# Performance work log

Measured on AMD Instinct MI355X. Metric: run time of the kernel, lower is better.

Reference implementation:

```python
import jax, jax.numpy as jnp
import numpy as np

U, P, D, H, E = 512, 1024, 128, 256, 98304
N = U + P


def setup_inputs() -> dict:
    key = jax.random.key(0)
    ks = jax.random.split(key, 16)
    def nrm(k, shape, scale=0.05):
        return jax.random.normal(k, shape, jnp.float32) * scale
    z = lambda *s: jnp.zeros(s, jnp.float32)
    return {
        "user_ids": jnp.arange(U),
        "paper_ids": jnp.arange(P),
        "edge_index": jax.random.randint(ks[0], (2, E), 0, N),
        "user_paper_interactions": jax.random.uniform(ks[1], (U, P), jnp.float32),
        "user_emb": nrm(ks[2], (U, D), 1.0),   # nn.Embedding tables
        "paper_emb": nrm(ks[3], (P, D), 1.0),
        "W0": nrm(ks[4], (D, H)), "b0": z(H),   # GCNConv weights (stored [in,out])
        "W1": nrm(ks[5], (H, H)), "b1": z(H),
        "W2": nrm(ks[6], (H, H)), "b2": z(H),
        "Wu": nrm(ks[7], (H, D)), "bu": z(D),   # user_output Linear
        "Wp": nrm(ks[8], (H, D)), "bp": z(D),   # paper_output Linear
        "Wq1": nrm(ks[9], (2 * D, H)), "bq1": z(H),  # predictor Linear 1
        "Wq2": nrm(ks[10], (H, 1)), "bq2": z(1),      # predictor Linear 2
    }


def gcn_conv(x, src, dst, W, b):
    """PyG GCNConv: add self-loops, symmetric D^-1/2 (A+I) D^-1/2 normalization."""
    n = x.shape[0]
    loop = jnp.arange(n)
    s = jnp.concatenate([src, loop])
    d = jnp.concatenate([dst, loop])
    deg = jax.ops.segment_sum(jnp.ones(d.shape, x.dtype), d, num_segments=n)
    dis = jnp.where(deg > 0, jax.lax.rsqrt(jnp.maximum(deg, 1.0)), 0.0)
    norm = dis[s] * dis[d]                      # [E+n]
    h = x @ W                                   # [n, H]
    out = jax.ops.segment_sum(h[s] * norm[:, None], d, num_segments=n)
    return out + b


def reference(user_ids, paper_ids, edge_index, user_paper_interactions,
              user_emb, paper_emb, W0, b0, W1, b1, W2, b2,
              Wu, bu, Wp, bp, Wq1, bq1, Wq2, bq2):
    # embedding lookups + node feature matrix [U+P, D]
    x = jnp.concatenate([user_emb[user_ids], paper_emb[paper_ids]], axis=0)
    src, dst = edge_index[0], edge_index[1]
    for W, b in ((W0, b0), (W1, b1), (W2, b2)):
        x = jax.nn.relu(gcn_conv(x, src, dst, W, b))  # dropout is identity in eval
    nu = user_ids.shape[0]
    np_ = paper_ids.shape[0]
    user_final = x[:nu] @ Wu + bu               # [U, D]
    paper_final = x[nu:] @ Wp + bp              # [P, D]
    # broadcast outer-product concat -> [U, P, 2D]
    combined = jnp.concatenate([
        jnp.broadcast_to(user_final[:, None, :], (nu, np_, user_final.shape[-1])),
        jnp.broadcast_to(paper_final[None, :, :], (nu, np_, paper_final.shape[-1])),
    ], axis=-1)
    h = jax.nn.relu(combined @ Wq1 + bq1)       # [U, P, H]
    pred = jax.nn.sigmoid(h @ Wq2 + bq2)[..., 0]  # [U, P]
    return pred
```

## Files before the change

kernel.cpp:

```cpp
#include <hip/hip_runtime.h>
#include <math.h>

constexpr int Uc = 512;
constexpr int Pc = 1024;
constexpr int Dc = 128;
constexpr int Hc = 256;
constexpr int Ec = 98304;
constexpr int Nc = 1536;
constexpr int CAP = 192;

__device__ __forceinline__ void fma4(float4& a, float n, const float4 r) {
    a.x += n * r.x; a.y += n * r.y; a.z += n * r.z; a.w += n * r.w;
}

template <int K>
__device__ __forceinline__ void gemm_core16(const float* __restrict__ xr,
                                            const float* __restrict__ wc, int M,
                                            float& acc0, float& acc1) {
#pragma unroll 4
    for (int k = 0; k < K; k += 4) {
        float4 a = *(const float4*)(xr + k);
        float2 b0 = *(const float2*)(wc + (size_t)k * M);
        float2 b1 = *(const float2*)(wc + (size_t)(k + 1) * M);
        float2 b2 = *(const float2*)(wc + (size_t)(k + 2) * M);
        float2 b3 = *(const float2*)(wc + (size_t)(k + 3) * M);
        acc0 += a.x * b0.x; acc1 += a.x * b0.y;
        acc0 += a.y * b1.x; acc1 += a.y * b1.y;
        acc0 += a.z * b2.x; acc1 += a.z * b2.y;
        acc0 += a.w * b3.x; acc1 += a.w * b3.y;
    }
}

__global__ void k_front(const int* __restrict__ e_src, const int* __restrict__ e_dst,
                        int* __restrict__ cnt, int* __restrict__ colF,
                        const float* __restrict__ Wu, const float* __restrict__ Wp,
                        const float* __restrict__ Wq1, const float* __restrict__ bu,
                        const float* __restrict__ bp, const float* __restrict__ bq1,
                        float* __restrict__ Wup, float* __restrict__ Wpp,
                        float* __restrict__ bvu, float* __restrict__ bvp) {
    int t = threadIdx.x, b = blockIdx.x;
    if (b < 384) {
        int e = b * 256 + t;
        int d = e_dst[e];
        int pos = atomicAdd(&cnt[d], 1);
        if (pos < CAP) colF[d * CAP + pos] = e_src[e];
    } else if (b < 640) {
        int id = b - 384;
        int z = id >> 7, tile = id & 127;
        int tx = t & 15, ty = t >> 4;
        const float* X = z ? Wp : Wu;
        const float* W = Wq1 + (z ? (size_t)Dc * Hc : 0);
        float* Y = z ? Wpp : Wup;
        int row = (tile >> 3) * 16 + ty, col = (tile & 7) * 32 + tx * 2;
        float a0 = 0.f, a1 = 0.f;
        gemm_core16<Dc>(X + (size_t)row * Dc, W + col, Hc, a0, a1);
        *(float2*)&Y[(size_t)row * Hc + col] = make_float2(a0, a1);
    } else if (b == 640) {
        float s = bq1[t];
#pragma unroll 8
        for (int d = 0; d < Dc; d++) s += bu[d] * Wq1[d * Hc + t];
        bvu[t] = s;
    } else {
        float s = 0.f;
#pragma unroll 8
        for (int d = 0; d < Dc; d++) s += bp[d] * Wq1[(Dc + d) * Hc + t];
        bvp[t] = s;
    }
}

__global__ void k_l0(const int* __restrict__ uid, const int* __restrict__ pid,
                     const float* __restrict__ ue, const float* __restrict__ pe,
                     const float* __restrict__ W0, const float* __restrict__ b0,
                     const int* __restrict__ cnt, const int* __restrict__ colF,
                     float* __restrict__ out) {
    __shared__ const float* sptr[4][CAP];
    __shared__ float snrm[4][CAP];
    __shared__ __align__(16) float agg[4][Dc];
    int t = threadIdx.x, b = blockIdx.x;
    int ibase = b * 4;
    int c[4]; float di[4];
#pragma unroll
    for (int r = 0; r < 4; r++) {
        c[r] = cnt[ibase + r];
        di[r] = rsqrtf((float)(c[r] + 1));
        int deg = min(c[r], CAP);
        if (t < deg) {
            int s = colF[(ibase + r) * CAP + t];
            sptr[r][t] = (s < Uc) ? ue + (size_t)uid[s] * Dc
                                  : pe + (size_t)pid[s - Uc] * Dc;
            snrm[r][t] = rsqrtf((float)(cnt[s] + 1));
        }
    }
    __syncthreads();
    {
        int wv = t >> 6, ln = t & 63;
        int i = ibase + wv;
        int dg = min(c[wv], CAP);
        const float* xi = (i < Uc) ? ue + (size_t)uid[i] * Dc
                                   : pe + (size_t)pid[i - Uc] * Dc;
        float2 a2 = *(const float2*)(xi + ln * 2);
        float2 acc = make_float2(di[wv] * a2.x, di[wv] * a2.y);
        int j = 0;
        for (; j + 4 <= dg; j += 4) {
            float n0 = snrm[wv][j],     n1 = snrm[wv][j + 1];
            float n2 = snrm[wv][j + 2], n3 = snrm[wv][j + 3];
            float2 r0 = *(const float2*)(sptr[wv][j] + ln * 2);
            float2 r1 = *(const float2*)(sptr[wv][j + 1] + ln * 2);
            float2 r2 = *(const float2*)(sptr[wv][j + 2] + ln * 2);
            float2 r3 = *(const float2*)(sptr[wv][j + 3] + ln * 2);
            acc.x += n0 * r0.x + n1 * r1.x + n2 * r2.x + n3 * r3.x;
            acc.y += n0 * r0.y + n1 * r1.y + n2 * r2.y + n3 * r3.y;
        }
        for (; j < dg; j++) {
            float2 r0 = *(const float2*)(sptr[wv][j] + ln * 2);
            acc.x += snrm[wv][j] * r0.x;
            acc.y += snrm[wv][j] * r0.y;
        }
        agg[wv][ln * 2]     = di[wv] * acc.x;
        agg[wv][ln * 2 + 1] = di[wv] * acc.y;
    }
    __syncthreads();
    float a0 = 0.f, a1 = 0.f, a2 = 0.f, a3 = 0.f;
#pragma unroll 2
    for (int k = 0; k < Dc; k += 4) {
        float4 g0 = *(const float4*)&agg[0][k];
        float4 g1 = *(const float4*)&agg[1][k];
        float4 g2 = *(const float4*)&agg[2][k];
        float4 g3 = *(const float4*)&agg[3][k];
        float w0 = W0[(size_t)(k + 0) * Hc + t];
        float w1 = W0[(size_t)(k + 1) * Hc + t];
        float w2 = W0[(size_t)(k + 2) * Hc + t];
        float w3 = W0[(size_t)(k + 3) * Hc + t];
        a0 += g0.x * w0 + g0.y * w1 + g0.z * w2 + g0.w * w3;
        a1 += g1.x * w0 + g1.y * w1 + g1.z * w2 + g1.w * w3;
        a2 += g2.x * w0 + g2.y * w1 + g2.z * w2 + g2.w * w3;
        a3 += g3.x * w0 + g3.y * w1 + g3.z * w2 + g3.w * w3;
    }
    float bb = b0[t];
    out[(size_t)(ibase + 0) * Hc + t] = fmaxf(a0 + bb, 0.f);
    out[(size_t)(ibase + 1) * Hc + t] = fmaxf(a1 + bb, 0.f);
    out[(size_t)(ibase + 2) * Hc + t] = fmaxf(a2 + bb, 0.f);
    out[(size_t)(ibase + 3) * Hc + t] = fmaxf(a3 + bb, 0.f);
}

__device__ __forceinline__ void agg_wave(const float* __restrict__ X,
                                         const int (*sidx)[CAP], const float (*snrm)[CAP],
                                         const int* c, const float* di, int ibase,
                                         float (*agg)[Hc], int t) {
    int wv = t >> 6, ln = t & 63;
    int dg = min(c[wv], CAP);
    float4 acc = *(const float4*)&X[(size_t)(ibase + wv) * Hc + ln * 4];
    acc.x *= di[wv]; acc.y *= di[wv]; acc.z *= di[wv]; acc.w *= di[wv];
    int j = 0;
    for (; j + 4 <= dg; j += 4) {
        float n0 = snrm[wv][j],     n1 = snrm[wv][j + 1];
        float n2 = snrm[wv][j + 2], n3 = snrm[wv][j + 3];
        float4 r0 = *(const float4*)&X[sidx[wv][j]     + ln * 4];
        float4 r1 = *(const float4*)&X[sidx[wv][j + 1] + ln * 4];
        float4 r2 = *(const float4*)&X[sidx[wv][j + 2] + ln * 4];
        float4 r3 = *(const float4*)&X[sidx[wv][j + 3] + ln * 4];
        fma4(acc, n0, r0); fma4(acc, n1, r1); fma4(acc, n2, r2); fma4(acc, n3, r3);
    }
    for (; j < dg; j++) {
        float4 r0 = *(const float4*)&X[sidx[wv][j] + ln * 4];
        fma4(acc, snrm[wv][j], r0);
    }
    acc.x *= di[wv]; acc.y *= di[wv]; acc.z *= di[wv]; acc.w *= di[wv];
    *(float4*)&agg[wv][ln * 4] = acc;
}

__global__ void k_lh(const float* __restrict__ X, const float* __restrict__ W,
                     const float* __restrict__ bias, const int* __restrict__ cnt,
                     const int* __restrict__ colF, float* __restrict__ out) {
    __shared__ int sidx[4][CAP];
    __shared__ float snrm[4][CAP];
    __shared__ __align__(16) float agg[4][Hc];
    int t = threadIdx.x, b = blockIdx.x;
    int ibase = b * 4;
    int c[4]; float di[4];
#pragma unroll
    for (int r = 0; r < 4; r++) {
        c[r] = cnt[ibase + r];
        di[r] = rsqrtf((float)(c[r] + 1));
        int deg = min(c[r], CAP);
        if (t < deg) {
            int s = colF[(ibase + r) * CAP + t];
            sidx[r][t] = s * Hc;
            snrm[r][t] = rsqrtf((float)(cnt[s] + 1));
        }
    }
    __syncthreads();
    agg_wave(X, sidx, snrm, c, di, ibase, agg, t);
    __syncthreads();
    float a0 = 0.f, a1 = 0.f, a2 = 0.f, a3 = 0.f;
#pragma unroll 2
    for (int k = 0; k < Hc; k += 4) {
        float4 g0 = *(const float4*)&agg[0][k];
        float4 g1 = *(const float4*)&agg[1][k];
        float4 g2 = *(const float4*)&agg[2][k];
        float4 g3 = *(const float4*)&agg[3][k];
        float w0 = W[(size_t)(k + 0) * Hc + t];
        float w1 = W[(size_t)(k + 1) * Hc + t];
        float w2 = W[(size_t)(k + 2) * Hc + t];
        float w3 = W[(size_t)(k + 3) * Hc + t];
        a0 += g0.x * w0 + g0.y * w1 + g0.z * w2 + g0.w * w3;
        a1 += g1.x * w0 + g1.y * w1 + g1.z * w2 + g1.w * w3;
        a2 += g2.x * w0 + g2.y * w1 + g2.z * w2 + g2.w * w3;
        a3 += g3.x * w0 + g3.y * w1 + g3.z * w2 + g3.w * w3;
    }
    float bb = bias[t];
    out[(size_t)(ibase + 0) * Hc + t] = fmaxf(a0 + bb, 0.f);
    out[(size_t)(ibase + 1) * Hc + t] = fmaxf(a1 + bb, 0.f);
    out[(size_t)(ibase + 2) * Hc + t] = fmaxf(a2 + bb, 0.f);
    out[(size_t)(ibase + 3) * Hc + t] = fmaxf(a3 + bb, 0.f);
}

__global__ void k_lht(const float* __restrict__ X, const float* __restrict__ W2,
                      const float* __restrict__ b2, const int* __restrict__ cnt,
                      const int* __restrict__ colF,
                      const float* __restrict__ Wup, const float* __restrict__ Wpp,
                      const float* __restrict__ bvu, const float* __restrict__ bvp,
                      float* __restrict__ AuT, float* __restrict__ ApT) {
    __shared__ int sidx[4][CAP];
    __shared__ float snrm[4][CAP];
    __shared__ __align__(16) float agg[4][Hc];
    __shared__ __align__(16) float xloc[4][Hc];
    int t = threadIdx.x, b = blockIdx.x;
    int ibase = b * 4;
    int c[4]; float di[4];
#pragma unroll
    for (int r = 0; r < 4; r++) {
        c[r] = cnt[ibase + r];
        di[r] = rsqrtf((float)(c[r] + 1));
        int deg = min(c[r], CAP);
        if (t < deg) {
            int s = colF[(ibase + r) * CAP + t];
            sidx[r][t] = s * Hc;
            snrm[r][t] = rsqrtf((float)(cnt[s] + 1));
        }
    }
    __syncthreads();
    agg_wave(X, sidx, snrm, c, di, ibase, agg, t);
    __syncthreads();
    {
        float a0 = 0.f, a1 = 0.f, a2 = 0.f, a3 = 0.f;
#pragma unroll 2
        for (int k = 0; k < Hc; k += 4) {
            float4 g0 = *(const float4*)&agg[0][k];
            float4 g1 = *(const float4*)&agg[1][k];
            float4 g2 = *(const float4*)&agg[2][k];
            float4 g3 = *(const float4*)&agg[3][k];
            float w0 = W2[(size_t)(k + 0) * Hc + t];
            float w1 = W2[(size_t)(k + 1) * Hc + t];
            float w2 = W2[(size_t)(k + 2) * Hc + t];
            float w3 = W2[(size_t)(k + 3) * Hc + t];
            a0 += g0.x * w0 + g0.y * w1 + g0.z * w2 + g0.w * w3;
            a1 += g1.x * w0 + g1.y * w1 + g1.z * w2 + g1.w * w3;
            a2 += g2.x * w0 + g2.y * w1 + g2.z * w2 + g2.w * w3;
            a3 += g3.x * w0 + g3.y * w1 + g3.z * w2 + g3.w * w3;
        }
        float bb = b2[t];
        xloc[0][t] = fmaxf(a0 + bb, 0.f);
        xloc[1][t] = fmaxf(a1 + bb, 0.f);
        xloc[2][t] = fmaxf(a2 + bb, 0.f);
        xloc[3][t] = fmaxf(a3 + bb, 0.f);
    }
    __syncthreads();
    {
        const float* Wsel = (b < 128) ? Wup : Wpp;
        const float* bsel = (b < 128) ? bvu : bvp;
        float* YT  = (b < 128) ? AuT : ApT;
        int ldy    = (b < 128) ? Uc : Pc;
        int rloc   = (b < 128) ? ibase : ibase - Uc;
        float a0 = 0.f, a1 = 0.f, a2 = 0.f, a3 = 0.f;
#pragma unroll 2
        for (int k = 0; k < Hc; k += 4) {
            float4 g0 = *(const float4*)&xloc[0][k];
            float4 g1 = *(const float4*)&xloc[1][k];
            float4 g2 = *(const float4*)&xloc[2][k];
            float4 g3 = *(const float4*)&xloc[3][k];
            float w0 = Wsel[(size_t)(k + 0) * Hc + t];
            float w1 = Wsel[(size_t)(k + 1) * Hc + t];
            float w2 = Wsel[(size_t)(k + 2) * Hc + t];
            float w3 = Wsel[(size_t)(k + 3) * Hc + t];
            a0 += g0.x * w0 + g0.y * w1 + g0.z * w2 + g0.w * w3;
            a1 += g1.x * w0 + g1.y * w1 + g1.z * w2 + g1.w * w3;
            a2 += g2.x * w0 + g2.y * w1 + g2.z * w2 + g2.w * w3;
            a3 += g3.x * w0 + g3.y * w1 + g3.z * w2 + g3.w * w3;
        }
        float bb = bsel[t];
        float4 o = make_float4(a0 + bb, a1 + bb, a2 + bb, a3 + bb);
        *(float4*)&YT[(size_t)t * ldy + rloc] = o;
    }
}

__global__ void k_pred(const float* __restrict__ AuT, const float* __restrict__ ApT,
                       const float* __restrict__ Wq2, const float* __restrict__ bq2,
                       float* __restrict__ out) {
    __shared__ float auS[Hc * 16];
    int t = threadIdx.x;
    int ub = blockIdx.x * 16, pb = blockIdx.y * 64;
#pragma unroll
    for (int i = t; i < Hc * 16; i += 256) {
        int k = i >> 4, u = i & 15;
        auS[i] = AuT[(size_t)k * Uc + ub + u];
    }
    __syncthreads();
    int uu = t >> 5;
    int pp = t & 31;
    const float* app = ApT + pb + pp * 2;
    const float* aup = auS + uu * 2;
    float acc[2][2] = {};
#pragma unroll 4
    for (int k = 0; k < Hc; k += 4) {
        float4 wv = *(const float4*)&Wq2[k];
        float2 a[4], p2[4];
#pragma unroll
        for (int j = 0; j < 4; j++) a[j] = *(const float2*)(aup + (k + j) * 16);
#pragma unroll
        for (int j = 0; j < 4; j++) p2[j] = *(const float2*)(app + (size_t)(k + j) * Pc);
        const float* w = (const float*)&wv;
#pragma unroll
        for (int j = 0; j < 4; j++) {
            float a0 = a[j].x, a1 = a[j].y;
            float p0 = p2[j].x, p1 = p2[j].y;
            acc[0][0] += fmaxf(a0 + p0, 0.f) * w[j];
            acc[0][1] += fmaxf(a0 + p1, 0.f) * w[j];
            acc[1][0] += fmaxf(a1 + p0, 0.f) * w[j];
            acc[1][1] += fmaxf(a1 + p1, 0.f) * w[j];
        }
    }
    float bq = bq2[0];
#pragma unroll
    for (int r = 0; r < 2; r++) {
        int u = ub + uu * 2 + r;
        float2 o;
        o.x = 1.f / (1.f + __expf(-(acc[r][0] + bq)));
        o.y = 1.f / (1.f + __expf(-(acc[r][1] + bq)));
        *(float2*)&out[(size_t)u * Pc + pb + pp * 2] = o;
    }
}


extern "C" void kernel_launch(void* const* d_in, const int* in_sizes, int n_in,
                              void* d_out, int out_size, void* d_ws, size_t ws_size,
                              hipStream_t stream) {
    const int*   uid = (const int*)d_in[0];
    const int*   pid = (const int*)d_in[1];
    const int*   ei  = (const int*)d_in[2];
    const float* ue  = (const float*)d_in[4];
    const float* pe  = (const float*)d_in[5];
    const float* W0  = (const float*)d_in[6];  const float* b0 = (const float*)d_in[7];
    const float* W1  = (const float*)d_in[8];  const float* b1 = (const float*)d_in[9];
    const float* W2  = (const float*)d_in[10]; const float* b2 = (const float*)d_in[11];
    const float* Wu  = (const float*)d_in[12]; const float* bu = (const float*)d_in[13];
    const float* Wp  = (const float*)d_in[14]; const float* bp = (const float*)d_in[15];
    const float* Wq1 = (const float*)d_in[16]; const float* bq1 = (const float*)d_in[17];
    const float* Wq2 = (const float*)d_in[18]; const float* bq2 = (const float*)d_in[19];

    const int* e_src = ei;
    const int* e_dst = ei + Ec;

    char* w = (char*)d_ws;
    auto alloc = [&](size_t bytes) { char* p = w; w += (bytes + 255) & ~size_t(255); return p; };
    int*   cnt  = (int*)alloc(Nc * 4);
    int*   colF = (int*)alloc((size_t)Nc * CAP * 4);
    float* xA   = (float*)alloc((size_t)Nc * Hc * 4);
    float* xB   = (float*)alloc((size_t)Nc * Hc * 4);
    float* Wup  = (float*)alloc((size_t)Hc * Hc * 4);
    float* Wpp  = (float*)alloc((size_t)Hc * Hc * 4);
    float* bvu  = (float*)alloc(Hc * 4);
    float* bvp  = (float*)alloc(Hc * 4);
    float* AuT  = (float*)alloc((size_t)Hc * Uc * 4);
    float* ApT  = (float*)alloc((size_t)Hc * Pc * 4);
    float* pred = (float*)d_out;

    hipMemsetAsync(cnt, 0, Nc * 4, stream);
    k_front<<<642, 256, 0, stream>>>(e_src, e_dst, cnt, colF, Wu, Wp, Wq1,
                                     bu, bp, bq1, Wup, Wpp, bvu, bvp);
    k_l0<<<Nc / 4, 256, 0, stream>>>(uid, pid, ue, pe, W0, b0, cnt, colF, xA);
    k_lh<<<Nc / 4, 256, 0, stream>>>(xA, W1, b1, cnt, colF, xB);
    k_lht<<<Nc / 4, 256, 0, stream>>>(xB, W2, b2, cnt, colF, Wup, Wpp, bvu, bvp, AuT, ApT);
    k_pred<<<dim3(Uc / 16, Pc / 64), 256, 0, stream>>>(AuT, ApT, Wq2, bq2, pred);
}
```

Measured before the change: 204.1 us.

## Split neighbor aggregation across two waves per node, halve nodes per block

GCN layer kernels now process two nodes per block instead of four, with two waves splitting each node's neighbor list and reducing partial sums through shared memory. This doubles the block count and the waves in flight for the latency-bound gather. In exchange, weight rows are reused across fewer nodes in the fused GEMM, and an extra shared-memory reduction and barrier are added.

```diff
diff --git a/kernel.cpp b/kernel.cpp
--- a/kernel.cpp
+++ b/kernel.cpp
@@ -73,14 +73,15 @@
                      const float* __restrict__ W0, const float* __restrict__ b0,
                      const int* __restrict__ cnt, const int* __restrict__ colF,
                      float* __restrict__ out) {
-    __shared__ const float* sptr[4][CAP];
-    __shared__ float snrm[4][CAP];
-    __shared__ __align__(16) float agg[4][Dc];
+    __shared__ const float* sptr[2][CAP];
+    __shared__ float snrm[2][CAP];
+    __shared__ __align__(16) float pagg[4][Dc];
+    __shared__ __align__(16) float agg[2][Dc];
     int t = threadIdx.x, b = blockIdx.x;
-    int ibase = b * 4;
-    int c[4]; float di[4];
-#pragma unroll
-    for (int r = 0; r < 4; r++) {
+    int ibase = b * 2;
+    int c[2]; float di[2];
+#pragma unroll
+    for (int r = 0; r < 2; r++) {
         c[r] = cnt[ibase + r];
         di[r] = rsqrtf((float)(c[r] + 1));
         int deg = min(c[r], CAP);
@@ -94,92 +95,104 @@
     __syncthreads();
     {
         int wv = t >> 6, ln = t & 63;
-        int i = ibase + wv;
-        int dg = min(c[wv], CAP);
-        const float* xi = (i < Uc) ? ue + (size_t)uid[i] * Dc
-                                   : pe + (size_t)pid[i - Uc] * Dc;
-        float2 a2 = *(const float2*)(xi + ln * 2);
-        float2 acc = make_float2(di[wv] * a2.x, di[wv] * a2.y);
-        int j = 0;
-        for (; j + 4 <= dg; j += 4) {
-            float n0 = snrm[wv][j],     n1 = snrm[wv][j + 1];
-            float n2 = snrm[wv][j + 2], n3 = snrm[wv][j + 3];
-            float2 r0 = *(const float2*)(sptr[wv][j] + ln * 2);
-            float2 r1 = *(const float2*)(sptr[wv][j + 1] + ln * 2);
-            float2 r2 = *(const float2*)(sptr[wv][j + 2] + ln * 2);
-            float2 r3 = *(const float2*)(sptr[wv][j + 3] + ln * 2);
+        int r = wv >> 1, h = wv & 1;
+        int i = ibase + r;
+        int dg = min(c[r], CAP);
+        int dg2 = dg >> 1;
+        int j0 = h ? dg2 : 0, j1 = h ? dg : dg2;
+        float2 acc = make_float2(0.f, 0.f);
+        if (h == 0) {
+            const float* xi = (i < Uc) ? ue + (size_t)uid[i] * Dc
+                                       : pe + (size_t)pid[i - Uc] * Dc;
+            float2 a2 = *(const float2*)(xi + ln * 2);
+            acc.x = di[r] * a2.x;
+            acc.y = di[r] * a2.y;
+        }
+        int j = j0;
+        for (; j + 4 <= j1; j += 4) {
+            float n0 = snrm[r][j],     n1 = snrm[r][j + 1];
+            float n2 = snrm[r][j + 2], n3 = snrm[r][j + 3];
+            float2 r0 = *(const float2*)(sptr[r][j] + ln * 2);
+            float2 r1 = *(const float2*)(sptr[r][j + 1] + ln * 2);
+            float2 r2 = *(const float2*)(sptr[r][j + 2] + ln * 2);
+            float2 r3 = *(const float2*)(sptr[r][j + 3] + ln * 2);
             acc.x += n0 * r0.x + n1 * r1.x + n2 * r2.x + n3 * r3.x;
             acc.y += n0 * r0.y + n1 * r1.y + n2 * r2.y + n3 * r3.y;
         }
-        for (; j < dg; j++) {
-            float2 r0 = *(const float2*)(sptr[wv][j] + ln * 2);
-            acc.x += snrm[wv][j] * r0.x;
-            acc.y += snrm[wv][j] * r0.y;
-        }
-        agg[wv][ln * 2]     = di[wv] * acc.x;
-        agg[wv][ln * 2 + 1] = di[wv] * acc.y;
-    }
-    __syncthreads();
-    float a0 = 0.f, a1 = 0.f, a2 = 0.f, a3 = 0.f;
+        for (; j < j1; j++) {
+            float2 r0 = *(const float2*)(sptr[r][j] + ln * 2);
+            acc.x += snrm[r][j] * r0.x;
+            acc.y += snrm[r][j] * r0.y;
+        }
+        pagg[wv][ln * 2]     = acc.x;
+        pagg[wv][ln * 2 + 1] = acc.y;
+    }
+    __syncthreads();
+    {
+        int r = t >> 7, f = t & 127;
+        agg[r][f] = di[r] * (pagg[2 * r][f] + pagg[2 * r + 1][f]);
+    }
+    __syncthreads();
+    float a0 = 0.f, a1 = 0.f;
 #pragma unroll 2
     for (int k = 0; k < Dc; k += 4) {
         float4 g0 = *(const float4*)&agg[0][k];
         float4 g1 = *(const float4*)&agg[1][k];
-        float4 g2 = *(const float4*)&agg[2][k];
-        float4 g3 = *(const float4*)&agg[3][k];
         float w0 = W0[(size_t)(k + 0) * Hc + t];
         float w1 = W0[(size_t)(k + 1) * Hc + t];
         float w2 = W0[(size_t)(k + 2) * Hc + t];
         float w3 = W0[(size_t)(k + 3) * Hc + t];
         a0 += g0.x * w0 + g0.y * w1 + g0.z * w2 + g0.w * w3;
         a1 += g1.x * w0 + g1.y * w1 + g1.z * w2 + g1.w * w3;
-        a2 += g2.x * w0 + g2.y * w1 + g2.z * w2 + g2.w * w3;
-        a3 += g3.x * w0 + g3.y * w1 + g3.z * w2 + g3.w * w3;
     }
     float bb = b0[t];
     out[(size_t)(ibase + 0) * Hc + t] = fmaxf(a0 + bb, 0.f);
     out[(size_t)(ibase + 1) * Hc + t] = fmaxf(a1 + bb, 0.f);
-    out[(size_t)(ibase + 2) * Hc + t] = fmaxf(a2 + bb, 0.f);
-    out[(size_t)(ibase + 3) * Hc + t] = fmaxf(a3 + bb, 0.f);
-}
-
-__device__ __forceinline__ void agg_wave(const float* __restrict__ X,
-                                         const int (*sidx)[CAP], const float (*snrm)[CAP],
-                                         const int* c, const float* di, int ibase,
-                                         float (*agg)[Hc], int t) {
+}
+
+__device__ __forceinline__ void agg_wave2(const float* __restrict__ X,
+                                          const int (*sidx)[CAP], const float (*snrm)[CAP],
+                                          const int* c, const float* di, int ibase,
+                                          float (*pagg)[Hc], int t) {
     int wv = t >> 6, ln = t & 63;
-    int dg = min(c[wv], CAP);
-    float4 acc = *(const float4*)&X[(size_t)(ibase + wv) * Hc + ln * 4];
-    acc.x *= di[wv]; acc.y *= di[wv]; acc.z *= di[wv]; acc.w *= di[wv];
-    int j = 0;
-    for (; j + 4 <= dg; j += 4) {
-        float n0 = snrm[wv][j],     n1 = snrm[wv][j + 1];
-        float n2 = snrm[wv][j + 2], n3 = snrm[wv][j + 3];
-        float4 r0 = *(const float4*)&X[sidx[wv][j]     + ln * 4];
-        float4 r1 = *(const float4*)&X[sidx[wv][j + 1] + ln * 4];
-        float4 r2 = *(const float4*)&X[sidx[wv][j + 2] + ln * 4];
-        float4 r3 = *(const float4*)&X[sidx[wv][j + 3] + ln * 4];
+    int r = wv >> 1, h = wv & 1;
+    int dg = min(c[r], CAP);
+    int dg2 = dg >> 1;
+    int j0 = h ? dg2 : 0, j1 = h ? dg : dg2;
+    float4 acc = make_float4(0.f, 0.f, 0.f, 0.f);
+    if (h == 0) {
+        acc = *(const float4*)&X[(size_t)(ibase + r) * Hc + ln * 4];
+        acc.x *= di[r]; acc.y *= di[r]; acc.z *= di[r]; acc.w *= di[r];
+    }
+    int j = j0;
+    for (; j + 4 <= j1; j += 4) {
+        float n0 = snrm[r][j],     n1 = snrm[r][j + 1];
+        float n2 = snrm[r][j + 2], n3 = snrm[r][j + 3];
+        float4 r0 = *(const float4*)&X[sidx[r][j]     + ln * 4];
+        float4 r1 = *(const float4*)&X[sidx[r][j + 1] + ln * 4];
+        float4 r2 = *(const float4*)&X[sidx[r][j + 2] + ln * 4];
+        float4 r3 = *(const float4*)&X[sidx[r][j + 3] + ln * 4];
         fma4(acc, n0, r0); fma4(acc, n1, r1); fma4(acc, n2, r2); fma4(acc, n3, r3);
     }
-    for (; j < dg; j++) {
-        float4 r0 = *(const float4*)&X[sidx[wv][j] + ln * 4];
-        fma4(acc, snrm[wv][j], r0);
-    }
-    acc.x *= di[wv]; acc.y *= di[wv]; acc.z *= di[wv]; acc.w *= di[wv];
-    *(float4*)&agg[wv][ln * 4] = acc;
+    for (; j < j1; j++) {
+        float4 r0 = *(const float4*)&X[sidx[r][j] + ln * 4];
+        fma4(acc, snrm[r][j], r0);
+    }
+    *(float4*)&pagg[wv][ln * 4] = acc;
 }
 
 __global__ void k_lh(const float* __restrict__ X, const float* __restrict__ W,
                      const float* __restrict__ bias, const int* __restrict__ cnt,
                      const int* __restrict__ colF, float* __restrict__ out) {
-    __shared__ int sidx[4][CAP];
-    __shared__ float snrm[4][CAP];
-    __shared__ __align__(16) float agg[4][Hc];
+    __shared__ int sidx[2][CAP];
+    __shared__ float snrm[2][CAP];
+    __shared__ __align__(16) float pagg[4][Hc];
+    __shared__ __align__(16) float agg[2][Hc];
     int t = threadIdx.x, b = blockIdx.x;
-    int ibase = b * 4;
-    int c[4]; float di[4];
-#pragma unroll
-    for (int r = 0; r < 4; r++) {
+    int ibase = b * 2;
+    int c[2]; float di[2];
+#pragma unroll
+    for (int r = 0; r < 2; r++) {
         c[r] = cnt[ibase + r];
         di[r] = rsqrtf((float)(c[r] + 1));
         int deg = min(c[r], CAP);
@@ -190,29 +203,26 @@
         }
     }
     __syncthreads();
-    agg_wave(X, sidx, snrm, c, di, ibase, agg, t);
-    __syncthreads();
-    float a0 = 0.f, a1 = 0.f, a2 = 0.f, a3 = 0.f;
+    agg_wave2(X, sidx, snrm, c, di, ibase, pagg, t);
+    __syncthreads();
+    agg[0][t] = di[0] * (pagg[0][t] + pagg[1][t]);
+    agg[1][t] = di[1] * (pagg[2][t] + pagg[3][t]);
+    __syncthreads();
+    float a0 = 0.f, a1 = 0.f;
 #pragma unroll 2
     for (int k = 0; k < Hc; k += 4) {
         float4 g0 = *(const float4*)&agg[0][k];
         float4 g1 = *(const float4*)&agg[1][k];
-        float4 g2 = *(const float4*)&agg[2][k];
-        float4 g3 = *(const float4*)&agg[3][k];
         float w0 = W[(size_t)(k + 0) * Hc + t];
         float w1 = W[(size_t)(k + 1) * Hc + t];
         float w2 = W[(size_t)(k + 2) * Hc + t];
         float w3 = W[(size_t)(k + 3) * Hc + t];
         a0 += g0.x * w0 + g0.y * w1 + g0.z * w2 + g0.w * w3;
         a1 += g1.x * w0 + g1.y * w1 + g1.z * w2 + g1.w * w3;
-        a2 += g2.x * w0 + g2.y * w1 + g2.z * w2 + g2.w * w3;
-        a3 += g3.x * w0 + g3.y * w1 + g3.z * w2 + g3.w * w3;
     }
     float bb = bias[t];
     out[(size_t)(ibase + 0) * Hc + t] = fmaxf(a0 + bb, 0.f);
     out[(size_t)(ibase + 1) * Hc + t] = fmaxf(a1 + bb, 0.f);
-    out[(size_t)(ibase + 2) * Hc + t] = fmaxf(a2 + bb, 0.f);
-    out[(size_t)(ibase + 3) * Hc + t] = fmaxf(a3 + bb, 0.f);
 }
 
 __global__ void k_lht(const float* __restrict__ X, const float* __restrict__ W2,
@@ -221,15 +231,16 @@
                       const float* __restrict__ Wup, const float* __restrict__ Wpp,
                       const float* __restrict__ bvu, const float* __restrict__ bvp,
                       float* __restrict__ AuT, float* __restrict__ ApT) {
-    __shared__ int sidx[4][CAP];
-    __shared__ float snrm[4][CAP];
-    __shared__ __align__(16) float agg[4][Hc];
-    __shared__ __align__(16) float xloc[4][Hc];
+    __shared__ int sidx[2][CAP];
+    __shared__ float snrm[2][CAP];
+    __shared__ __align__(16) float pagg[4][Hc];
+    __shared__ __align__(16) float agg[2][Hc];
+    __shared__ __align__(16) float xloc[2][Hc];
     int t = threadIdx.x, b = blockIdx.x;
-    int ibase = b * 4;
-    int c[4]; float di[4];
-#pragma unroll
-    for (int r = 0; r < 4; r++) {
+    int ibase = b * 2;
+    int c[2]; float di[2];
+#pragma unroll
+    for (int r = 0; r < 2; r++) {
         c[r] = cnt[ibase + r];
         di[r] = rsqrtf((float)(c[r] + 1));
         int deg = min(c[r], CAP);
@@ -240,57 +251,49 @@
         }
     }
     __syncthreads();
-    agg_wave(X, sidx, snrm, c, di, ibase, agg, t);
+    agg_wave2(X, sidx, snrm, c, di, ibase, pagg, t);
+    __syncthreads();
+    agg[0][t] = di[0] * (pagg[0][t] + pagg[1][t]);
+    agg[1][t] = di[1] * (pagg[2][t] + pagg[3][t]);
     __syncthreads();
     {
-        float a0 = 0.f, a1 = 0.f, a2 = 0.f, a3 = 0.f;
+        float a0 = 0.f, a1 = 0.f;
 #pragma unroll 2
         for (int k = 0; k < Hc; k += 4) {
             float4 g0 = *(const float4*)&agg[0][k];
             float4 g1 = *(const float4*)&agg[1][k];
-            float4 g2 = *(const float4*)&agg[2][k];
-            float4 g3 = *(const float4*)&agg[3][k];
             float w0 = W2[(size_t)(k + 0) * Hc + t];
             float w1 = W2[(size_t)(k + 1) * Hc + t];
             float w2 = W2[(size_t)(k + 2) * Hc + t];
             float w3 = W2[(size_t)(k + 3) * Hc + t];
             a0 += g0.x * w0 + g0.y * w1 + g0.z * w2 + g0.w * w3;
             a1 += g1.x * w0 + g1.y * w1 + g1.z * w2 + g1.w * w3;
-            a2 += g2.x * w0 + g2.y * w1 + g2.z * w2 + g2.w * w3;
-            a3 += g3.x * w0 + g3.y * w1 + g3.z * w2 + g3.w * w3;
         }
         float bb = b2[t];
         xloc[0][t] = fmaxf(a0 + bb, 0.f);
         xloc[1][t] = fmaxf(a1 + bb, 0.f);
-        xloc[2][t] = fmaxf(a2 + bb, 0.f);
-        xloc[3][t] = fmaxf(a3 + bb, 0.f);
     }
     __syncthreads();
     {
-        const float* Wsel = (b < 128) ? Wup : Wpp;
-        const float* bsel = (b < 128) ? bvu : bvp;
-        float* YT  = (b < 128) ? AuT : ApT;
-        int ldy    = (b < 128) ? Uc : Pc;
-        int rloc   = (b < 128) ? ibase : ibase - Uc;
-        float a0 = 0.f, a1 = 0.f, a2 = 0.f, a3 = 0.f;
+        const float* Wsel = (b < 256) ? Wup : Wpp;
+        const float* bsel = (b < 256) ? bvu : bvp;
+        float* YT  = (b < 256) ? AuT : ApT;
+        int ldy    = (b < 256) ? Uc : Pc;
+        int rloc   = (b < 256) ? ibase : ibase - Uc;
+        float a0 = 0.f, a1 = 0.f;
 #pragma unroll 2
         for (int k = 0; k < Hc; k += 4) {
             float4 g0 = *(const float4*)&xloc[0][k];
             float4 g1 = *(const float4*)&xloc[1][k];
-            float4 g2 = *(const float4*)&xloc[2][k];
-            float4 g3 = *(const float4*)&xloc[3][k];
             float w0 = Wsel[(size_t)(k + 0) * Hc + t];
             float w1 = Wsel[(size_t)(k + 1) * Hc + t];
             float w2 = Wsel[(size_t)(k + 2) * Hc + t];
             float w3 = Wsel[(size_t)(k + 3) * Hc + t];
             a0 += g0.x * w0 + g0.y * w1 + g0.z * w2 + g0.w * w3;
             a1 += g1.x * w0 + g1.y * w1 + g1.z * w2 + g1.w * w3;
-            a2 += g2.x * w0 + g2.y * w1 + g2.z * w2 + g2.w * w3;
-            a3 += g3.x * w0 + g3.y * w1 + g3.z * w2 + g3.w * w3;
         }
         float bb = bsel[t];
-        float4 o = make_float4(a0 + bb, a1 + bb, a2 + bb, a3 + bb);
-        *(float4*)&YT[(size_t)t * ldy + rloc] = o;
+        *(float2*)&YT[(size_t)t * ldy + rloc] = make_float2(a0 + bb, a1 + bb);
     }
 }
 
@@ -378,8 +381,8 @@
     hipMemsetAsync(cnt, 0, Nc * 4, stream);
     k_front<<<642, 256, 0, stream>>>(e_src, e_dst, cnt, colF, Wu, Wp, Wq1,
                                      bu, bp, bq1, Wup, Wpp, bvu, bvp);
-    k_l0<<<Nc / 4, 256, 0, stream>>>(uid, pid, ue, pe, W0, b0, cnt, colF, xA);
-    k_lh<<<Nc / 4, 256, 0, stream>>>(xA, W1, b1, cnt, colF, xB);
-    k_lht<<<Nc / 4, 256, 0, stream>>>(xB, W2, b2, cnt, colF, Wup, Wpp, bvu, bvp, AuT, ApT);
+    k_l0<<<Nc / 2, 256, 0, stream>>>(uid, pid, ue, pe, W0, b0, cnt, colF, xA);
+    k_lh<<<Nc / 2, 256, 0, stream>>>(xA, W1, b1, cnt, colF, xB);
+    k_lht<<<Nc / 2, 256, 0, stream>>>(xB, W2, b2, cnt, colF, Wup, Wpp, bvu, bvp, AuT, ApT);
     k_pred<<<dim3(Uc / 16, Pc / 64), 256, 0, stream>>>(AuT, ApT, Wq2, bq2, pred);
 }
```

After: 193.2 us. -5.3%, faster.
